# Kernel tuning notes

Hardware: AMD Instinct MI355X
Metric: run time of the kernel (lower is better)

The kernel has to match this reference:

```python
import jax, jax.numpy as jnp
import numpy as np

D_MODEL = 2048
NUM_HEADS = 16
FAN = 4
HEAD = D_MODEL // NUM_HEADS
EPS = 1e-5


def _layernorm(x):
    # LayerNorm over last dim, no affine params (elementwise_affine=False)
    mu = jnp.mean(x, axis=-1, keepdims=True)
    var = jnp.mean(jnp.square(x - mu), axis=-1, keepdims=True)
    return (x - mu) * jax.lax.rsqrt(var + EPS)


def setup_inputs() -> dict:
    key = jax.random.key(0)
    k0, k1, k2, k3, k4 = jax.random.split(key, 5)
    B, T = 2, 2048
    qkv_out = 3 * D_MODEL + FAN * D_MODEL  # 14336
    s_in = 1.0 / np.sqrt(D_MODEL)
    s_h = 1.0 / np.sqrt(FAN * D_MODEL)
    return {
        "inputs": jax.random.normal(k0, (B, T, D_MODEL), dtype=jnp.float32),
        "W_qkv": jax.random.normal(k1, (D_MODEL, qkv_out), dtype=jnp.float32) * s_in,
        "b_qkv": jax.random.normal(k2, (qkv_out,), dtype=jnp.float32) * 0.01,
        "W_mlp": jax.random.normal(k3, (FAN * D_MODEL, D_MODEL), dtype=jnp.float32) * s_h,
        "b_mlp": jax.random.normal(k4, (D_MODEL,), dtype=jnp.float32) * 0.01,
    }


def reference(inputs, W_qkv, b_qkv, W_mlp, b_mlp):
    B, T, C = inputs.shape
    # parallel QKV + MLP hidden projection on pre-LN input
    x = _layernorm(inputs)
    qkv_hidden = jnp.einsum("btc,cf->btf", x, W_qkv) + b_qkv
    q = qkv_hidden[..., :D_MODEL]
    k = qkv_hidden[..., D_MODEL:2 * D_MODEL]
    v = qkv_hidden[..., 2 * D_MODEL:3 * D_MODEL]
    hidden = qkv_hidden[..., 3 * D_MODEL:]

    # split heads: (B, H, T, head)
    def to_heads(t):
        return t.reshape(B, T, NUM_HEADS, HEAD).transpose(0, 2, 1, 3)

    q = _layernorm(to_heads(q))  # QK-LayerNorm over head dim
    k = _layernorm(to_heads(k))
    v = to_heads(v)

    # MLP branch (exact GELU, torch default)
    mlp_out = jnp.einsum("bth,hc->btc", jax.nn.gelu(hidden, approximate=False), W_mlp) + b_mlp

    # causal attention
    logits = jnp.einsum("bhqd,bhkd->bhqk", q, k) * (HEAD ** -0.5)
    causal = jnp.tril(jnp.ones((T, T), dtype=bool))
    logits = jnp.where(causal, logits, -jnp.inf)
    scores = jax.nn.softmax(logits, axis=-1)
    outs = jnp.einsum("bhqk,bhkd->bhqd", scores, v)
    outs = outs.transpose(0, 2, 1, 3).reshape(B, T, C)

    return outs + mlp_out + inputs
```

## Files before the change

kernel.cpp:

```cpp
#include <hip/hip_runtime.h>
#include <hip/hip_bf16.h>
#include <math.h>

typedef __bf16 bf16;
typedef __bf16 bf16x4 __attribute__((ext_vector_type(4)));
typedef __bf16 bf16x8 __attribute__((ext_vector_type(8)));
typedef unsigned short u16x8 __attribute__((ext_vector_type(8)));
typedef float f32x4 __attribute__((ext_vector_type(4)));

#define MFMA16(a, b, c) __builtin_amdgcn_mfma_f32_16x16x32_bf16((a), (b), (c), 0, 0, 0)

__device__ __forceinline__ void llds16(const void* g, void* l) {
  __builtin_amdgcn_global_load_lds(
      (const __attribute__((address_space(1))) unsigned*)g,
      (__attribute__((address_space(3))) unsigned*)l, 16, 0, 0);
}

__global__ __launch_bounds__(256) void transpose_cvt(const float* __restrict__ src,
                                                     bf16* __restrict__ dst, int R, int C) {
  __shared__ float tile[32][33];
  const int bx = blockIdx.x * 32, by = blockIdx.y * 32;
  const int tx = threadIdx.x, ty = threadIdx.y;
#pragma unroll
  for (int i = 0; i < 32; i += 8)
    tile[ty + i][tx] = src[(size_t)(by + ty + i) * C + bx + tx];
  __syncthreads();
#pragma unroll
  for (int i = 0; i < 32; i += 8)
    dst[(size_t)(bx + ty + i) * R + by + tx] = (bf16)tile[tx][ty + i];
}

__global__ __launch_bounds__(256) void ln_rows(const float* __restrict__ x,
                                               bf16* __restrict__ y) {
  const int r = blockIdx.x, t = threadIdx.x;
  const float* xr = x + (size_t)r * 2048;
  f32x4 a = ((const f32x4*)xr)[t];
  f32x4 b = ((const f32x4*)xr)[t + 256];
  float s = 0.f, ss = 0.f;
#pragma unroll
  for (int j = 0; j < 4; ++j) {
    s += a[j] + b[j];
    ss += a[j] * a[j] + b[j] * b[j];
  }
#pragma unroll
  for (int m = 1; m < 64; m <<= 1) {
    s += __shfl_xor(s, m, 64);
    ss += __shfl_xor(ss, m, 64);
  }
  __shared__ float red[8];
  const int wv = t >> 6;
  if ((t & 63) == 0) { red[wv] = s; red[4 + wv] = ss; }
  __syncthreads();
  s = red[0] + red[1] + red[2] + red[3];
  ss = red[4] + red[5] + red[6] + red[7];
  const float mu = s * (1.f / 2048.f);
  const float var = ss * (1.f / 2048.f) - mu * mu;
  const float rs = rsqrtf(var + 1e-5f);
  bf16x4 o1, o2;
#pragma unroll
  for (int j = 0; j < 4; ++j) {
    o1[j] = (bf16)((a[j] - mu) * rs);
    o2[j] = (bf16)((b[j] - mu) * rs);
  }
  bf16* yr = y + (size_t)r * 2048;
  ((bf16x4*)yr)[t] = o1;
  ((bf16x4*)yr)[t + 256] = o2;
}

template <int MODE>
__global__ __launch_bounds__(256) void gemm_bt(const bf16* __restrict__ A,
                                               const bf16* __restrict__ B,
                                               void* __restrict__ Cp, int K, int lda,
                                               int ldb, int ldc,
                                               const float* __restrict__ bias,
                                               const float* __restrict__ res1,
                                               const float* __restrict__ res2) {
  __shared__ bf16 As[128 * 64];
  __shared__ bf16 Bs[128 * 64];
  const int t = threadIdx.x, w = t >> 6, l = t & 63;
  const int l16 = l & 15, lg = l >> 4;
  const int wm = w >> 1, wn = w & 1;
  const int m0 = blockIdx.y * 128, n0 = blockIdx.x * 128;
  const int arow = l >> 3, acol = (l & 7) * 8;
  f32x4 acc[4][4] = {};
  for (int k0 = 0; k0 < K; k0 += 64) {
    __syncthreads();
#pragma unroll
    for (int i = 0; i < 4; ++i) {
      const int c = i * 4 + w;
      const int row = c * 8 + arow;
      llds16(A + (size_t)(m0 + row) * lda + k0 + acol, (char*)As + c * 1024 + l * 16);
      llds16(B + (size_t)(n0 + row) * ldb + k0 + acol, (char*)Bs + c * 1024 + l * 16);
    }
    __syncthreads();
#pragma unroll
    for (int ks = 0; ks < 2; ++ks) {
      bf16x8 af[4], bfr[4];
#pragma unroll
      for (int mi = 0; mi < 4; ++mi)
        af[mi] = *(const bf16x8*)(As + (wm * 64 + mi * 16 + l16) * 64 + ks * 32 + lg * 8);
#pragma unroll
      for (int ni = 0; ni < 4; ++ni)
        bfr[ni] = *(const bf16x8*)(Bs + (wn * 64 + ni * 16 + l16) * 64 + ks * 32 + lg * 8);
#pragma unroll
      for (int mi = 0; mi < 4; ++mi)
#pragma unroll
        for (int ni = 0; ni < 4; ++ni)
          acc[mi][ni] = MFMA16(af[mi], bfr[ni], acc[mi][ni]);
    }
  }
  const int crow0 = m0 + wm * 64 + lg * 4;
  const int ccol0 = n0 + wn * 64 + l16;
  if (MODE == 0) {
    bf16* C = (bf16*)Cp;
#pragma unroll
    for (int mi = 0; mi < 4; ++mi)
#pragma unroll
      for (int ni = 0; ni < 4; ++ni) {
        const int col = ccol0 + ni * 16;
        const float bv = bias[col];
#pragma unroll
        for (int r = 0; r < 4; ++r)
          C[(size_t)(crow0 + mi * 16 + r) * ldc + col] = (bf16)(acc[mi][ni][r] + bv);
      }
  } else {
    float* C = (float*)Cp;
#pragma unroll
    for (int mi = 0; mi < 4; ++mi)
#pragma unroll
      for (int ni = 0; ni < 4; ++ni) {
        const int col = ccol0 + ni * 16;
        const float bv = bias[col];
#pragma unroll
        for (int r = 0; r < 4; ++r) {
          const size_t idx = (size_t)(crow0 + mi * 16 + r) * ldc + col;
          C[idx] = acc[mi][ni][r] + bv + res1[idx] + res2[idx];
        }
      }
  }
}

__global__ __launch_bounds__(256) void post1(bf16* __restrict__ qkv) {
  const int r = blockIdx.x, t = threadIdx.x, w = t >> 6, l = t & 63;
  bf16* row = qkv + (size_t)r * 14336;
#pragma unroll
  for (int gi = 0; gi < 8; ++gi) {
    const int g = w + gi * 4;
    bf16* p = row + g * 128 + l * 2;
    const float a = (float)p[0], b = (float)p[1];
    float s = a + b, ss = a * a + b * b;
#pragma unroll
    for (int m = 1; m < 64; m <<= 1) {
      s += __shfl_xor(s, m, 64);
      ss += __shfl_xor(ss, m, 64);
    }
    const float mu = s * (1.f / 128.f);
    const float var = ss * (1.f / 128.f) - mu * mu;
    const float rs = rsqrtf(var + 1e-5f);
    p[0] = (bf16)((a - mu) * rs);
    p[1] = (bf16)((b - mu) * rs);
  }
  bf16* hb = row + 6144;
#pragma unroll
  for (int i = 0; i < 8; ++i) {
    const int idx = t + i * 256;
    bf16x4 v = ((bf16x4*)hb)[idx];
#pragma unroll
    for (int j = 0; j < 4; ++j) {
      float f = (float)v[j];
      f = 0.5f * f * (1.f + erff(f * 0.70710678118f));
      v[j] = (bf16)f;
    }
    ((bf16x4*)hb)[idx] = v;
  }
}

__global__ __launch_bounds__(256) void attn_kernel(const bf16* __restrict__ qkv,
                                                   float* __restrict__ attn_out) {
  __shared__ bf16 K_lds[32][136];
  __shared__ bf16 V_lds[128][40];
  __shared__ bf16 P_lds[4][16][40];
  const int t = threadIdx.x, w = t >> 6, l = t & 63;
  const int l16 = l & 15, lg = l >> 4;
  const int b = blockIdx.y >> 4, h = blockIdx.y & 15;
  const int qb0 = blockIdx.x * 64;
  const int tq0 = qb0 + w * 16;
  const size_t bT = (size_t)b * 2048;
  const int LDQ = 14336;
  const size_t qoff = (size_t)h * 128;
  const size_t koff = 2048 + (size_t)h * 128;
  const size_t voff = 4096 + (size_t)h * 128;
  const float SCALE = 0.08838834764831845f;

  bf16x8 qf[4];
  {
    const bf16* qrow = qkv + (bT + tq0 + l16) * LDQ + qoff + lg * 8;
#pragma unroll
    for (int dc = 0; dc < 4; ++dc) qf[dc] = *(const bf16x8*)(qrow + dc * 32);
  }
  float m_r[4], l_r[4];
  f32x4 accO[8] = {};
#pragma unroll
  for (int r = 0; r < 4; ++r) { m_r[r] = -1e30f; l_r[r] = 0.f; }

  const int nkv = (qb0 >> 5) + 2;
  for (int kt = 0; kt < nkv; ++kt) {
    const int kt0 = kt << 5;
    __syncthreads();
#pragma unroll
    for (int it = 0; it < 2; ++it) {
      const int c = it * 256 + t;
      const int krow = c >> 4, c8 = (c & 15) * 8;
      *(bf16x8*)(&K_lds[krow][c8]) =
          *(const bf16x8*)(qkv + (bT + kt0 + krow) * LDQ + koff + c8);
    }
    {
      const int kp = (t & 15) * 2, dg = (t >> 4) * 8;
      const bf16* g0 = qkv + (bT + kt0 + kp) * LDQ + voff + dg;
      u16x8 v0 = *(const u16x8*)g0;
      u16x8 v1 = *(const u16x8*)(g0 + LDQ);
#pragma unroll
      for (int j = 0; j < 8; ++j) {
        const unsigned pk = (unsigned)v0[j] | ((unsigned)v1[j] << 16);
        *(unsigned*)(&V_lds[dg + j][kp]) = pk;
      }
    }
    __syncthreads();
    if (kt0 <= tq0 + 15) {
      f32x4 sacc[2] = {};
#pragma unroll
      for (int dc = 0; dc < 4; ++dc) {
        bf16x8 kf = *(const bf16x8*)(&K_lds[l16][dc * 32 + lg * 8]);
        sacc[0] = MFMA16(qf[dc], kf, sacc[0]);
      }
#pragma unroll
      for (int dc = 0; dc < 4; ++dc) {
        bf16x8 kf = *(const bf16x8*)(&K_lds[16 + l16][dc * 32 + lg * 8]);
        sacc[1] = MFMA16(qf[dc], kf, sacc[1]);
      }
      float s0[4], s1[4];
      const bool need_mask = (kt0 + 31 > tq0);
#pragma unroll
      for (int r = 0; r < 4; ++r) {
        s0[r] = sacc[0][r] * SCALE;
        s1[r] = sacc[1][r] * SCALE;
      }
      if (need_mask) {
#pragma unroll
        for (int r = 0; r < 4; ++r) {
          const int q = tq0 + lg * 4 + r;
          if (kt0 + l16 > q) s0[r] = -1e30f;
          if (kt0 + 16 + l16 > q) s1[r] = -1e30f;
        }
      }
      float pmax[4];
#pragma unroll
      for (int r = 0; r < 4; ++r) pmax[r] = fmaxf(s0[r], s1[r]);
#pragma unroll
      for (int m = 1; m < 16; m <<= 1)
#pragma unroll
        for (int r = 0; r < 4; ++r) pmax[r] = fmaxf(pmax[r], __shfl_xor(pmax[r], m, 64));
      float fr[4];
#pragma unroll
      for (int r = 0; r < 4; ++r) {
        const float mn = fmaxf(m_r[r], pmax[r]);
        fr[r] = __expf(m_r[r] - mn);
        m_r[r] = mn;
      }
      float p0[4], p1[4], rsum[4];
#pragma unroll
      for (int r = 0; r < 4; ++r) {
        p0[r] = __expf(s0[r] - m_r[r]);
        p1[r] = __expf(s1[r] - m_r[r]);
        rsum[r] = p0[r] + p1[r];
      }
#pragma unroll
      for (int m = 1; m < 16; m <<= 1)
#pragma unroll
        for (int r = 0; r < 4; ++r) rsum[r] += __shfl_xor(rsum[r], m, 64);
#pragma unroll
      for (int r = 0; r < 4; ++r) l_r[r] = l_r[r] * fr[r] + rsum[r];
#pragma unroll
      for (int f = 0; f < 8; ++f)
#pragma unroll
        for (int r = 0; r < 4; ++r) accO[f][r] *= fr[r];
#pragma unroll
      for (int r = 0; r < 4; ++r) {
        P_lds[w][lg * 4 + r][l16] = (bf16)p0[r];
        P_lds[w][lg * 4 + r][16 + l16] = (bf16)p1[r];
      }
      bf16x8 pa = *(const bf16x8*)(&P_lds[w][l16][lg * 8]);
#pragma unroll
      for (int f = 0; f < 8; ++f) {
        bf16x8 vf = *(const bf16x8*)(&V_lds[f * 16 + l16][lg * 8]);
        accO[f] = MFMA16(pa, vf, accO[f]);
      }
    }
  }
  float inv[4];
#pragma unroll
  for (int r = 0; r < 4; ++r) inv[r] = 1.0f / l_r[r];
  float* orow = attn_out + (bT + tq0 + lg * 4) * 2048 + (size_t)h * 128 + l16;
#pragma unroll
  for (int f = 0; f < 8; ++f)
#pragma unroll
    for (int r = 0; r < 4; ++r) orow[(size_t)r * 2048 + f * 16] = accO[f][r] * inv[r];
}

extern "C" void kernel_launch(void* const* d_in, const int* in_sizes, int n_in,
                              void* d_out, int out_size, void* d_ws, size_t ws_size,
                              hipStream_t stream) {
  const float* inputs = (const float*)d_in[0];
  const float* W_qkv = (const float*)d_in[1];
  const float* b_qkv = (const float*)d_in[2];
  const float* W_mlp = (const float*)d_in[3];
  const float* b_mlp = (const float*)d_in[4];
  float* out = (float*)d_out;

  char* ws = (char*)d_ws;
  bf16* Wqkv_t = (bf16*)ws;
  bf16* Wmlp_t = (bf16*)(ws + 58720256);
  bf16* x_ln = (bf16*)(ws + 92274688);
  bf16* qkv = (bf16*)(ws + 109051904);
  float* attn = (float*)(ws + 226492416);

  transpose_cvt<<<dim3(14336 / 32, 2048 / 32), dim3(32, 8), 0, stream>>>(W_qkv, Wqkv_t,
                                                                         2048, 14336);
  transpose_cvt<<<dim3(2048 / 32, 8192 / 32), dim3(32, 8), 0, stream>>>(W_mlp, Wmlp_t,
                                                                        8192, 2048);
  ln_rows<<<4096, 256, 0, stream>>>(inputs, x_ln);
  gemm_bt<0><<<dim3(112, 32), 256, 0, stream>>>(x_ln, Wqkv_t, qkv, 2048, 2048, 2048,
                                                14336, b_qkv, nullptr, nullptr);
  post1<<<4096, 256, 0, stream>>>(qkv);
  attn_kernel<<<dim3(32, 32), 256, 0, stream>>>(qkv, attn);
  gemm_bt<1><<<dim3(16, 32), 256, 0, stream>>>(qkv + 6144, Wmlp_t, out, 8192, 14336,
                                               8192, 2048, b_mlp, inputs, attn);
}
```

Measured before the change: 1.120 ms.

## Replace GEMM with 256-row tiled, 4-stage pipelined 8-wave kernel

Replaces the 128x128 single-buffered GEMM with a 512-thread kernel using 256xBN tiles, a 4-deep LDS ring of async global-to-LDS loads with explicit vmcnt waits, XOR-swizzled LDS layout, and a remapped block order for L2 locality. It also raises MFMA priority during compute phases. The goal is to hide global-load latency behind MFMA work and raise arithmetic intensity per block. In exchange it uses more LDS and registers, and the MLP GEMM launches only 256 blocks, which may leave CUs underutilized.

```diff
diff --git a/kernel.cpp b/kernel.cpp
--- a/kernel.cpp
+++ b/kernel.cpp
@@ -67,76 +67,123 @@
   ((bf16x4*)yr)[t + 256] = o2;
 }
 
-template <int MODE>
-__global__ __launch_bounds__(256) void gemm_bt(const bf16* __restrict__ A,
-                                               const bf16* __restrict__ B,
-                                               void* __restrict__ Cp, int K, int lda,
-                                               int ldb, int ldc,
-                                               const float* __restrict__ bias,
-                                               const float* __restrict__ res1,
-                                               const float* __restrict__ res2) {
-  __shared__ bf16 As[128 * 64];
-  __shared__ bf16 Bs[128 * 64];
+template <int MODE, int BN>
+__global__ __launch_bounds__(512, 2) void gemm8p(
+    const bf16* __restrict__ A, const bf16* __restrict__ B, void* __restrict__ Cp,
+    const int K, const int lda, const int ldb, const int ldc,
+    const float* __restrict__ bias, const float* __restrict__ res1,
+    const float* __restrict__ res2, const int gx) {
+  constexpr int WN = BN / 4;
+  constexpr int NR = WN / 16;
+  constexpr int NRH = NR / 2;
+  constexpr int NLB = BN / 128;
+  constexpr int BUFSZ = 8192 + NLB * 4096;
+  __shared__ bf16 lds[4 * BUFSZ];
+
   const int t = threadIdx.x, w = t >> 6, l = t & 63;
   const int l16 = l & 15, lg = l >> 4;
-  const int wm = w >> 1, wn = w & 1;
-  const int m0 = blockIdx.y * 128, n0 = blockIdx.x * 128;
-  const int arow = l >> 3, acol = (l & 7) * 8;
-  f32x4 acc[4][4] = {};
-  for (int k0 = 0; k0 < K; k0 += 64) {
-    __syncthreads();
-#pragma unroll
-    for (int i = 0; i < 4; ++i) {
-      const int c = i * 4 + w;
-      const int row = c * 8 + arow;
-      llds16(A + (size_t)(m0 + row) * lda + k0 + acol, (char*)As + c * 1024 + l * 16);
-      llds16(B + (size_t)(n0 + row) * ldb + k0 + acol, (char*)Bs + c * 1024 + l * 16);
-    }
-    __syncthreads();
-#pragma unroll
-    for (int ks = 0; ks < 2; ++ks) {
-      bf16x8 af[4], bfr[4];
-#pragma unroll
-      for (int mi = 0; mi < 4; ++mi)
-        af[mi] = *(const bf16x8*)(As + (wm * 64 + mi * 16 + l16) * 64 + ks * 32 + lg * 8);
-#pragma unroll
-      for (int ni = 0; ni < 4; ++ni)
-        bfr[ni] = *(const bf16x8*)(Bs + (wn * 64 + ni * 16 + l16) * 64 + ks * 32 + lg * 8);
-#pragma unroll
-      for (int mi = 0; mi < 4; ++mi)
-#pragma unroll
-        for (int ni = 0; ni < 4; ++ni)
-          acc[mi][ni] = MFMA16(af[mi], bfr[ni], acc[mi][ni]);
-    }
-  }
-  const int crow0 = m0 + wm * 64 + lg * 4;
-  const int ccol0 = n0 + wn * 64 + l16;
-  if (MODE == 0) {
+  const int wm = w >> 2, wn = w & 3;
+  const int nwg = gridDim.x;
+  const int id = (blockIdx.x & 7) * (nwg >> 3) + (blockIdx.x >> 3);
+  const int by = id / gx, bx = id - by * gx;
+  const int m0 = by * 256, n0 = bx * BN;
+  const int NT = K >> 5;
+
+  auto stage = [&](int kt) {
+    bf16* Ab = lds + (size_t)(kt & 3) * BUFSZ;
+    bf16* Bb = Ab + 8192;
+    const int k0 = kt << 5;
+    const int r4 = t >> 2;
+    const int cg = (t & 3) ^ ((t >> 3) & 3);
+#pragma unroll
+    for (int j = 0; j < 2; ++j)
+      llds16(A + (size_t)(m0 + j * 128 + r4) * lda + k0 + cg * 8, Ab + j * 4096 + t * 8);
+#pragma unroll
+    for (int j = 0; j < NLB; ++j)
+      llds16(B + (size_t)(n0 + j * 128 + r4) * ldb + k0 + cg * 8, Bb + j * 4096 + t * 8);
+  };
+
+  f32x4 acc[8][NR] = {};
+  stage(0); stage(1); stage(2);
+  if constexpr (BN == 256) asm volatile("s_waitcnt vmcnt(8)" ::: "memory");
+  else                     asm volatile("s_waitcnt vmcnt(6)" ::: "memory");
+  __builtin_amdgcn_s_barrier();
+
+  const int arow = wm * 128 + l16;
+  const int brow = wn * WN + l16;
+  const int slot = (lg ^ ((l16 >> 1) & 3)) * 8;
+
+  for (int kt = 0; kt < NT; ++kt) {
+    const bf16* Ab = lds + (size_t)(kt & 3) * BUFSZ;
+    const bf16* Bb = Ab + 8192;
+    if (kt + 3 < NT) stage(kt + 3);
+    bf16x8 af[8], bfr[NR];
+#pragma unroll
+    for (int mi = 0; mi < 8; ++mi)
+      af[mi] = *(const bf16x8*)(Ab + (arow + mi * 16) * 32 + slot);
+#pragma unroll
+    for (int ni = 0; ni < NRH; ++ni)
+      bfr[ni] = *(const bf16x8*)(Bb + (brow + ni * 16) * 32 + slot);
+    __builtin_amdgcn_s_setprio(1);
+#pragma unroll
+    for (int mi = 0; mi < 8; ++mi)
+#pragma unroll
+      for (int ni = 0; ni < NRH; ++ni)
+        acc[mi][ni] = MFMA16(af[mi], bfr[ni], acc[mi][ni]);
+    __builtin_amdgcn_s_setprio(0);
+#pragma unroll
+    for (int ni = NRH; ni < NR; ++ni)
+      bfr[ni] = *(const bf16x8*)(Bb + (brow + ni * 16) * 32 + slot);
+    __builtin_amdgcn_s_setprio(1);
+#pragma unroll
+    for (int mi = 0; mi < 8; ++mi)
+#pragma unroll
+      for (int ni = NRH; ni < NR; ++ni)
+        acc[mi][ni] = MFMA16(af[mi], bfr[ni], acc[mi][ni]);
+    __builtin_amdgcn_s_setprio(0);
+    if (kt < NT - 1) {
+      const int staged = (kt + 3 < NT) ? kt + 3 : NT - 1;
+      const int infl = staged - (kt + 1);
+      if (infl >= 2) {
+        if constexpr (BN == 256) asm volatile("s_waitcnt vmcnt(8)" ::: "memory");
+        else                     asm volatile("s_waitcnt vmcnt(6)" ::: "memory");
+      } else if (infl == 1) {
+        if constexpr (BN == 256) asm volatile("s_waitcnt vmcnt(4)" ::: "memory");
+        else                     asm volatile("s_waitcnt vmcnt(3)" ::: "memory");
+      } else {
+        asm volatile("s_waitcnt vmcnt(0)" ::: "memory");
+      }
+      __builtin_amdgcn_s_barrier();
+    }
+  }
+
+  const int crow0 = m0 + wm * 128 + lg * 4;
+  const int ccol0 = n0 + wn * WN + l16;
+  if constexpr (MODE == 0) {
     bf16* C = (bf16*)Cp;
 #pragma unroll
-    for (int mi = 0; mi < 4; ++mi)
-#pragma unroll
-      for (int ni = 0; ni < 4; ++ni) {
-        const int col = ccol0 + ni * 16;
-        const float bv = bias[col];
+    for (int ni = 0; ni < NR; ++ni) {
+      const float bv = bias[ccol0 + ni * 16];
+#pragma unroll
+      for (int mi = 0; mi < 8; ++mi)
 #pragma unroll
         for (int r = 0; r < 4; ++r)
-          C[(size_t)(crow0 + mi * 16 + r) * ldc + col] = (bf16)(acc[mi][ni][r] + bv);
-      }
+          C[(size_t)(crow0 + mi * 16 + r) * ldc + ccol0 + ni * 16] =
+              (bf16)(acc[mi][ni][r] + bv);
+    }
   } else {
     float* C = (float*)Cp;
 #pragma unroll
-    for (int mi = 0; mi < 4; ++mi)
-#pragma unroll
-      for (int ni = 0; ni < 4; ++ni) {
-        const int col = ccol0 + ni * 16;
-        const float bv = bias[col];
+    for (int ni = 0; ni < NR; ++ni) {
+      const float bv = bias[ccol0 + ni * 16];
+#pragma unroll
+      for (int mi = 0; mi < 8; ++mi)
 #pragma unroll
         for (int r = 0; r < 4; ++r) {
-          const size_t idx = (size_t)(crow0 + mi * 16 + r) * ldc + col;
+          const size_t idx = (size_t)(crow0 + mi * 16 + r) * ldc + ccol0 + ni * 16;
           C[idx] = acc[mi][ni][r] + bv + res1[idx] + res2[idx];
         }
-      }
+    }
   }
 }
 
@@ -329,10 +376,10 @@
   transpose_cvt<<<dim3(2048 / 32, 8192 / 32), dim3(32, 8), 0, stream>>>(W_mlp, Wmlp_t,
                                                                         8192, 2048);
   ln_rows<<<4096, 256, 0, stream>>>(inputs, x_ln);
-  gemm_bt<0><<<dim3(112, 32), 256, 0, stream>>>(x_ln, Wqkv_t, qkv, 2048, 2048, 2048,
-                                                14336, b_qkv, nullptr, nullptr);
+  gemm8p<0, 256><<<896, 512, 0, stream>>>(x_ln, Wqkv_t, qkv, 2048, 2048, 2048, 14336,
+                                          b_qkv, nullptr, nullptr, 56);
   post1<<<4096, 256, 0, stream>>>(qkv);
   attn_kernel<<<dim3(32, 32), 256, 0, stream>>>(qkv, attn);
-  gemm_bt<1><<<dim3(16, 32), 256, 0, stream>>>(qkv + 6144, Wmlp_t, out, 8192, 14336,
-                                               8192, 2048, b_mlp, inputs, attn);
-}
+  gemm8p<1, 128><<<256, 512, 0, stream>>>(qkv + 6144, Wmlp_t, out, 8192, 14336, 8192,
+                                          2048, b_mlp, inputs, attn, 16);
+}
```

Result: faster. 960.4 us (-14.3%).
